# Kernel optimization log

Hardware: AMD Instinct MI355X
Metric: run time of the kernel (lower is better)

Reference implementation:

```python
import jax, jax.numpy as jnp
import numpy as np


def _gcn_conv(x, edge_index, W, b):
    # PyG GCNConv: h = x @ W; out = D^{-1/2}(A+I)D^{-1/2} h + b
    N = x.shape[0]
    src, dst = edge_index[0], edge_index[1]
    # degree with self-loops (edge weights = 1)
    deg = jax.ops.segment_sum(jnp.ones(src.shape[0], x.dtype), dst, num_segments=N) + 1.0
    dis = jax.lax.rsqrt(deg)  # deg >= 1 so finite
    h = x @ W  # [N, F_out]
    norm = dis[src] * dis[dst]  # [E]
    msg = h[src] * norm[:, None]  # [E, F_out] -- dominant memory traffic
    agg = jax.ops.segment_sum(msg, dst, num_segments=N)
    # self-loop contribution: norm_ii = dis_i^2
    out = agg + h * (dis * dis)[:, None] + b
    return out


def setup_inputs() -> dict:
    key = jax.random.key(0)
    k1, k2, k3, k4, k5, k6 = jax.random.split(key, 6)
    N, E = 100000, 1600000
    in_ch, hid, out_ch = 256, 128, 64  # hid = 2*out_channels
    x = jax.random.normal(k1, (N, in_ch), dtype=jnp.float32)
    edge_index = jax.random.randint(k2, (2, E), 0, N, dtype=jnp.int64)
    # Glorot-style init for GCN weights, zero bias (PyG default)
    W1 = jax.random.normal(k3, (in_ch, hid), dtype=jnp.float32) / np.sqrt(in_ch)
    b1 = jnp.zeros((hid,), jnp.float32)
    W2 = jax.random.normal(k4, (hid, out_ch), dtype=jnp.float32) / np.sqrt(hid)
    b2 = jnp.zeros((out_ch,), jnp.float32)
    return {"x": x, "edge_index": edge_index, "W1": W1, "b1": b1, "W2": W2, "b2": b2}


def reference(x, edge_index, W1, b1, W2, b2):
    # Encoder.forward: k=2 layers of activation(GCNConv(x, edge_index))
    h = jax.nn.relu(_gcn_conv(x, edge_index, W1, b1))
    h = jax.nn.relu(_gcn_conv(h, edge_index, W2, b2))
    return h
```

## Files before the change

### kernel.cpp

```cpp
#include <hip/hip_runtime.h>
#include <math.h>

#define THREADS 256
#define HIST_ILP 8
#define EPB_SHIFT 11

static inline int cdiv(long long a, long long b) { return (int)((a + b - 1) / b); }

typedef __attribute__((ext_vector_type(8))) short bf16x8;
typedef __attribute__((ext_vector_type(4))) float f32x4;

__device__ inline unsigned f2bf_rne_u(float f) {
    unsigned u = __builtin_bit_cast(unsigned, f);
    return (u + 0x7FFFu + ((u >> 16) & 1u)) >> 16;
}
__device__ inline float bfu2f(unsigned h) {
    unsigned u = h << 16;
    return __builtin_bit_cast(float, u);
}


__device__ __forceinline__ void bfrag_unit(const float* __restrict__ W, short* __restrict__ frag,
                                           int NCT, int ctks, int lane) {
    int Nn = NCT * 16;
    int ct = ctks % NCT;
    int ks = ctks / NCT;
    int colc = ct * 16 + (lane & 15);
    int kbase = ks * 32 + (lane >> 4) * 8;
    short* base = frag + (size_t)ctks * 1024 + lane * 8;
    #pragma unroll
    for (int j = 0; j < 8; ++j) {
        float v = W[(size_t)(kbase + j) * Nn + colc];
        unsigned h = f2bf_rne_u(v);
        base[j] = (short)h;
        base[512 + j] = (short)f2bf_rne_u(v - bfu2f(h));
    }
}

__device__ __forceinline__ void hist8_body(const int* __restrict__ dst, int* __restrict__ deg8,
                                           int* __restrict__ rank, int E, int N,
                                           int hb, int copy) {
    int* deg = deg8 + (size_t)copy * N;
    const int chi = copy << 28;
    int base = (hb << EPB_SHIFT) + (int)threadIdx.x * HIST_ILP;
    if (base + HIST_ILP - 1 < E) {
        int4 d0 = *(const int4*)(dst + base);
        int4 d1 = *(const int4*)(dst + base + 4);
        int4 r0, r1;
        r0.x = atomicAdd(&deg[d0.x], 1) | chi;
        r0.y = atomicAdd(&deg[d0.y], 1) | chi;
        r0.z = atomicAdd(&deg[d0.z], 1) | chi;
        r0.w = atomicAdd(&deg[d0.w], 1) | chi;
        r1.x = atomicAdd(&deg[d1.x], 1) | chi;
        r1.y = atomicAdd(&deg[d1.y], 1) | chi;
        r1.z = atomicAdd(&deg[d1.z], 1) | chi;
        r1.w = atomicAdd(&deg[d1.w], 1) | chi;
        *(int4*)(rank + base) = r0;
        *(int4*)(rank + base + 4) = r1;
    } else {
        for (int e = base; e < E; ++e) rank[e] = atomicAdd(&deg[dst[e]], 1) | chi;
    }
}

__device__ __forceinline__ void fill_body(const int* __restrict__ src, const int* __restrict__ dst,
                                          const int* __restrict__ rank, const int* __restrict__ rp8,
                                          int* __restrict__ col, int E, int N, int blk) {
    int base = (blk * THREADS + (int)threadIdx.x) * 4;
    if (base + 3 < E) {
        int4 d = *(const int4*)(dst + base);
        int4 r = *(const int4*)(rank + base);
        int4 s = *(const int4*)(src + base);
        col[rp8[(size_t)(((unsigned)r.x) >> 28) * N + d.x] + (r.x & 0x0FFFFFFF)] = s.x;
        col[rp8[(size_t)(((unsigned)r.y) >> 28) * N + d.y] + (r.y & 0x0FFFFFFF)] = s.y;
        col[rp8[(size_t)(((unsigned)r.z) >> 28) * N + d.z] + (r.z & 0x0FFFFFFF)] = s.z;
        col[rp8[(size_t)(((unsigned)r.w) >> 28) * N + d.w] + (r.w & 0x0FFFFFFF)] = s.w;
    } else {
        for (int e = base; e < E; ++e) {
            int r = rank[e];
            col[rp8[(size_t)(((unsigned)r) >> 28) * N + dst[e]] + (r & 0x0FFFFFFF)] = src[e];
        }
    }
}

template<int NCT, int KS>
__device__ __forceinline__ void gemm_body(const float* __restrict__ A, const short* __restrict__ Bfrag,
                                          unsigned short* __restrict__ H, int M, int blk) {
    constexpr int K = KS * 32;
    constexpr int Nn = NCT * 16;
    const int lane = threadIdx.x & 63;
    const int wave = threadIdx.x >> 6;
    const int rowBase = blk * 128 + wave * 32;
    const int kgrp = (lane >> 4) * 8;

    const float* ap0;
    const float* ap1;
    {
        int r0 = rowBase + (lane & 15);      if (r0 >= M) r0 = M - 1;
        int r1 = rowBase + (lane & 15) + 16; if (r1 >= M) r1 = M - 1;
        ap0 = A + (size_t)r0 * K + kgrp;
        ap1 = A + (size_t)r1 * K + kgrp;
    }

    f32x4 acc[2][NCT] = {};

    float4 c00 = *(const float4*)(ap0);
    float4 c01 = *(const float4*)(ap0 + 4);
    float4 c10 = *(const float4*)(ap1);
    float4 c11 = *(const float4*)(ap1 + 4);

    for (int ks = 0; ks < KS; ++ks) {
        float4 n00, n01, n10, n11;
        if (ks + 1 < KS) {
            const float* p0 = ap0 + (size_t)(ks + 1) * 32;
            const float* p1 = ap1 + (size_t)(ks + 1) * 32;
            n00 = *(const float4*)(p0);
            n01 = *(const float4*)(p0 + 4);
            n10 = *(const float4*)(p1);
            n11 = *(const float4*)(p1 + 4);
        }
        bf16x8 ahi[2], alo[2];
        {
            float av0[8] = {c00.x, c00.y, c00.z, c00.w, c01.x, c01.y, c01.z, c01.w};
            float av1[8] = {c10.x, c10.y, c10.z, c10.w, c11.x, c11.y, c11.z, c11.w};
            #pragma unroll
            for (int j = 0; j < 8; ++j) {
                unsigned h0 = f2bf_rne_u(av0[j]);
                ahi[0][j] = (short)h0;
                alo[0][j] = (short)f2bf_rne_u(av0[j] - bfu2f(h0));
                unsigned h1 = f2bf_rne_u(av1[j]);
                ahi[1][j] = (short)h1;
                alo[1][j] = (short)f2bf_rne_u(av1[j] - bfu2f(h1));
            }
        }
        __builtin_amdgcn_s_setprio(1);
        #pragma unroll
        for (int ct = 0; ct < NCT; ++ct) {
            const short* bp = Bfrag + (size_t)(ks * NCT + ct) * 1024 + lane * 8;
            bf16x8 bhi = *(const bf16x8*)bp;
            bf16x8 blo = *(const bf16x8*)(bp + 512);
            #pragma unroll
            for (int t = 0; t < 2; ++t) {
                acc[t][ct] = __builtin_amdgcn_mfma_f32_16x16x32_bf16(ahi[t], bhi, acc[t][ct], 0, 0, 0);
                acc[t][ct] = __builtin_amdgcn_mfma_f32_16x16x32_bf16(ahi[t], blo, acc[t][ct], 0, 0, 0);
                acc[t][ct] = __builtin_amdgcn_mfma_f32_16x16x32_bf16(alo[t], bhi, acc[t][ct], 0, 0, 0);
            }
        }
        __builtin_amdgcn_s_setprio(0);
        c00 = n00; c01 = n01; c10 = n10; c11 = n11;
    }

    const int drow0 = rowBase + (lane >> 4) * 4;
    #pragma unroll
    for (int t = 0; t < 2; ++t) {
        #pragma unroll
        for (int r = 0; r < 4; ++r) {
            int row = drow0 + t * 16 + r;
            if (row < M) {
                unsigned short* hp = H + (size_t)row * Nn + (lane & 15);
                #pragma unroll
                for (int ct = 0; ct < NCT; ++ct)
                    hp[ct * 16] = (unsigned short)f2bf_rne_u(acc[t][ct][r]);
            }
        }
    }
}


__global__ __launch_bounds__(THREADS)
void zero_bfrag_kernel(int* __restrict__ deg8, int total8,
                       const float* __restrict__ W1, short* __restrict__ bf1,
                       const float* __restrict__ W2, short* __restrict__ bf2, int nbZero) {
    int b = (int)blockIdx.x;
    if (b < nbZero) {
        int base = (b * THREADS + (int)threadIdx.x) * 4;
        if (base + 3 < total8) {
            *(int4*)(deg8 + base) = make_int4(0, 0, 0, 0);
        } else {
            for (int i = base; i < total8; ++i) deg8[i] = 0;
        }
    } else {
        int u = (b - nbZero) * 4 + ((int)threadIdx.x >> 6);
        int lane = threadIdx.x & 63;
        if (u < 64) bfrag_unit(W1, bf1, 8, u, lane);
        else if (u < 80) bfrag_unit(W2, bf2, 4, u - 64, lane);
    }
}

__global__ __launch_bounds__(THREADS)
void hist_gemmA_kernel(const int* __restrict__ dst, int* __restrict__ deg8,
                       int* __restrict__ rank, int E, int N,
                       const float* __restrict__ A, const short* __restrict__ Bfrag,
                       unsigned short* __restrict__ H, int M,
                       int nbHist, int nbGemm) {
    int b = (int)blockIdx.x;
    int total = nbHist + nbGemm;
    long long t = (long long)b * nbGemm;
    int gBefore = (int)(t / total);
    bool isG = (((long long)(b + 1) * nbGemm) / total) > gBefore;
    if (isG) gemm_body<8, 8>(A, Bfrag, H, M, gBefore);
    else     hist8_body(dst, deg8, rank, E, N, b - gBefore, b & 7);
}

__global__ __launch_bounds__(THREADS)
void fill_gemmB_kernel(const int* __restrict__ src, const int* __restrict__ dst,
                       const int* __restrict__ rank, const int* __restrict__ rp8,
                       int* __restrict__ col, int E, int N,
                       const float* __restrict__ A, const short* __restrict__ Bfrag,
                       unsigned short* __restrict__ H, int M, int gemmOff,
                       int nbFill, int nbGemm) {
    int b = (int)blockIdx.x;
    int total = nbFill + nbGemm;
    long long t = (long long)b * nbGemm;
    int gBefore = (int)(t / total);
    bool isG = (((long long)(b + 1) * nbGemm) / total) > gBefore;
    if (isG) gemm_body<8, 8>(A, Bfrag, H, M, gemmOff + gBefore);
    else     fill_body(src, dst, rank, rp8, col, E, N, b - gBefore);
}

template<int NCT, int KS>
__global__ __launch_bounds__(THREADS)
void mfma_gemm_bf16out_kernel(const float* __restrict__ A, const short* __restrict__ Bfrag,
                              unsigned short* __restrict__ H, int M) {
    gemm_body<NCT, KS>(A, Bfrag, H, M, (int)blockIdx.x);
}


#define SCAN_BLOCK 256
#define SCAN_ITEMS 4

__global__ __launch_bounds__(SCAN_BLOCK)
void scan_block_kernel(const int* __restrict__ deg8, int* __restrict__ out,
                       int* __restrict__ blockSums, float* __restrict__ dis, int n) {
    __shared__ int sdata[SCAN_BLOCK];
    int base = blockIdx.x * (SCAN_BLOCK * SCAN_ITEMS);
    int tid = threadIdx.x;
    int v[SCAN_ITEMS];
    int sum = 0;
    #pragma unroll
    for (int k = 0; k < SCAN_ITEMS; ++k) {
        int idx = base + tid * SCAN_ITEMS + k;
        int s8 = 0;
        if (idx < n) {
            #pragma unroll
            for (int c = 0; c < 8; ++c) s8 += deg8[(size_t)c * n + idx];
            dis[idx] = rsqrtf((float)s8 + 1.0f);
        }
        v[k] = s8;
        sum += s8;
    }
    sdata[tid] = sum;
    __syncthreads();
    for (int off = 1; off < SCAN_BLOCK; off <<= 1) {
        int t = (tid >= off) ? sdata[tid - off] : 0;
        __syncthreads();
        sdata[tid] += t;
        __syncthreads();
    }
    if (tid == SCAN_BLOCK - 1) blockSums[blockIdx.x] = sdata[SCAN_BLOCK - 1];
    int run = (tid == 0) ? 0 : sdata[tid - 1];
    #pragma unroll
    for (int k = 0; k < SCAN_ITEMS; ++k) {
        int idx = base + tid * SCAN_ITEMS + k;
        if (idx < n) out[idx] = run;
        run += v[k];
    }
}

__global__ __launch_bounds__(SCAN_BLOCK)
void scan_sums_kernel(int* __restrict__ blockSums, int nB) {
    __shared__ int sdata[SCAN_BLOCK];
    int tid = threadIdx.x;
    sdata[tid] = (tid < nB) ? blockSums[tid] : 0;
    __syncthreads();
    for (int off = 1; off < SCAN_BLOCK; off <<= 1) {
        int t = (tid >= off) ? sdata[tid - off] : 0;
        __syncthreads();
        sdata[tid] += t;
        __syncthreads();
    }
    int excl = (tid == 0) ? 0 : sdata[tid - 1];
    if (tid < nB) blockSums[tid] = excl;
}

__global__ __launch_bounds__(SCAN_BLOCK)
void scan_add_rp8_kernel(int* __restrict__ rowptr, const int* __restrict__ blockSums,
                         const int* __restrict__ deg8, int* __restrict__ rp8,
                         int n, int E) {
    int base = blockIdx.x * (SCAN_BLOCK * SCAN_ITEMS);
    int add = blockSums[blockIdx.x];
    #pragma unroll
    for (int k = 0; k < SCAN_ITEMS; ++k) {
        int idx = base + threadIdx.x * SCAN_ITEMS + k;
        if (idx < n) {
            int val = rowptr[idx] + add;
            rowptr[idx] = val;
            int run = val;
            #pragma unroll
            for (int c = 0; c < 8; ++c) {
                rp8[(size_t)c * n + idx] = run;
                run += deg8[(size_t)c * n + idx];
            }
        }
    }
    if (blockIdx.x == 0 && threadIdx.x == 0) rowptr[n] = E;
}


__global__ __launch_bounds__(THREADS)
void gather_bf16_128_kernel(const unsigned short* __restrict__ g, const int* __restrict__ col,
                            const int* __restrict__ rowptr, const float* __restrict__ dis,
                            const float* __restrict__ bias, float* __restrict__ out, int N) {
    constexpr int F = 128;
    int wid = (int)((blockIdx.x * (long long)blockDim.x + threadIdx.x) >> 6);
    wid = __builtin_amdgcn_readfirstlane(wid);
    const int lane = threadIdx.x & 63;
    if (wid >= N) return;
    const float di = dis[wid];
    const int loff = lane * 2;

    float acc0 = 0.0f, acc1 = 0.0f;

    auto loadrow = [&](int s) -> unsigned {
        return *(const unsigned*)(g + (size_t)s * F + loff);
    };
    auto addconv = [&](unsigned u, float w) {
        acc0 += w * bfu2f(u & 0xFFFFu);
        acc1 += w * __builtin_bit_cast(float, u & 0xFFFF0000u);
    };

    addconv(loadrow(wid), di);

    int start = __builtin_amdgcn_readfirstlane(rowptr[wid]);
    int end   = __builtin_amdgcn_readfirstlane(rowptr[wid + 1]);
    const int* c = col + start;
    int rem = end - start;

    if (rem >= 4) {
        int s0 = __builtin_amdgcn_readfirstlane(c[0]);
        int s1 = __builtin_amdgcn_readfirstlane(c[1]);
        int s2 = __builtin_amdgcn_readfirstlane(c[2]);
        int s3 = __builtin_amdgcn_readfirstlane(c[3]);
        float w0 = dis[s0], w1 = dis[s1], w2 = dis[s2], w3 = dis[s3];
        unsigned u0 = loadrow(s0), u1 = loadrow(s1), u2 = loadrow(s2), u3 = loadrow(s3);
        c += 4; rem -= 4;
        while (rem >= 4) {
            int t0 = __builtin_amdgcn_readfirstlane(c[0]);
            int t1 = __builtin_amdgcn_readfirstlane(c[1]);
            int t2 = __builtin_amdgcn_readfirstlane(c[2]);
            int t3 = __builtin_amdgcn_readfirstlane(c[3]);
            float x0 = dis[t0], x1 = dis[t1], x2 = dis[t2], x3 = dis[t3];
            unsigned v0 = loadrow(t0), v1 = loadrow(t1), v2 = loadrow(t2), v3 = loadrow(t3);
            addconv(u0, w0); addconv(u1, w1); addconv(u2, w2); addconv(u3, w3);
            u0 = v0; u1 = v1; u2 = v2; u3 = v3;
            w0 = x0; w1 = x1; w2 = x2; w3 = x3;
            c += 4; rem -= 4;
        }
        addconv(u0, w0); addconv(u1, w1); addconv(u2, w2); addconv(u3, w3);
    }
    while (rem > 0) {
        int s = __builtin_amdgcn_readfirstlane(c[0]);
        addconv(loadrow(s), dis[s]);
        ++c; --rem;
    }

    float* orow = out + (size_t)wid * F + loff;
    float v0 = di * acc0 + bias[loff];
    float v1 = di * acc1 + bias[loff + 1];
    *(float2*)orow = make_float2(fmaxf(v0, 0.0f), fmaxf(v1, 0.0f));
}

__global__ __launch_bounds__(THREADS)
void gather_pair64_kernel(const unsigned short* __restrict__ g, const int* __restrict__ col,
                          const int* __restrict__ rowptr, const float* __restrict__ dis,
                          const float* __restrict__ bias, float* __restrict__ out, int N) {
    int wid = (int)((blockIdx.x * (long long)blockDim.x + threadIdx.x) >> 6);
    if (wid >= N) return;
    const int lane = threadIdx.x & 63;
    const int half = lane >> 5;
    const int cc = lane & 31;
    const float di = dis[wid];

    float acc0 = 0.0f, acc1 = 0.0f;

    auto loadrow = [&](int s) -> unsigned {
        return *(const unsigned*)(g + (size_t)s * 64 + cc * 2);
    };
    auto addconv = [&](unsigned u, float w) {
        acc0 += w * bfu2f(u & 0xFFFFu);
        acc1 += w * __builtin_bit_cast(float, u & 0xFFFF0000u);
    };

    addconv(loadrow(wid), half ? 0.0f : di);

    int start = rowptr[wid], end = rowptr[wid + 1];
    int j = start + half;
    int cnt = (j < end) ? ((end - j + 1) >> 1) : 0;

    if (cnt >= 4) {
        int s0 = col[j], s1 = col[j + 2], s2 = col[j + 4], s3 = col[j + 6];
        float w0 = dis[s0], w1 = dis[s1], w2 = dis[s2], w3 = dis[s3];
        unsigned u0 = loadrow(s0), u1 = loadrow(s1), u2 = loadrow(s2), u3 = loadrow(s3);
        j += 8; cnt -= 4;
        while (cnt >= 4) {
            int t0 = col[j], t1 = col[j + 2], t2 = col[j + 4], t3 = col[j + 6];
            float x0 = dis[t0], x1 = dis[t1], x2 = dis[t2], x3 = dis[t3];
            unsigned v0 = loadrow(t0), v1 = loadrow(t1), v2 = loadrow(t2), v3 = loadrow(t3);
            addconv(u0, w0); addconv(u1, w1); addconv(u2, w2); addconv(u3, w3);
            u0 = v0; u1 = v1; u2 = v2; u3 = v3;
            w0 = x0; w1 = x1; w2 = x2; w3 = x3;
            j += 8; cnt -= 4;
        }
        addconv(u0, w0); addconv(u1, w1); addconv(u2, w2); addconv(u3, w3);
    }
    while (cnt > 0) {
        int s = col[j];
        addconv(loadrow(s), dis[s]);
        j += 2; --cnt;
    }

    acc0 += __shfl_xor(acc0, 32);
    acc1 += __shfl_xor(acc1, 32);

    if (half == 0) {
        float v0 = fmaxf(di * acc0 + bias[cc * 2 + 0], 0.0f);
        float v1 = fmaxf(di * acc1 + bias[cc * 2 + 1], 0.0f);
        *(float2*)(out + (size_t)wid * 64 + cc * 2) = make_float2(v0, v1);
    }
}


#define BM 64
#define BN 64
#define BK 16

__global__ __launch_bounds__(THREADS)
void sgemm_kernel(const float* __restrict__ A, const float* __restrict__ B,
                  float* __restrict__ C, int M, int N, int K) {
    __shared__ float As[BK][BM + 1];
    __shared__ float Bs[BK][BN + 1];

    const int tid = threadIdx.x;
    const int tr = tid / 16;
    const int tc = tid % 16;
    const int rowBase = blockIdx.y * BM;
    const int colBase = blockIdx.x * BN;

    float acc[4][4] = {};

    for (int k0 = 0; k0 < K; k0 += BK) {
        #pragma unroll
        for (int i = tid; i < BM * BK; i += THREADS) {
            int r = i / BK, c = i % BK;
            int gr = rowBase + r;
            As[c][r] = (gr < M) ? A[(size_t)gr * K + k0 + c] : 0.0f;
        }
        #pragma unroll
        for (int i = tid; i < BK * BN; i += THREADS) {
            int r = i / BN, c = i % BN;
            Bs[r][c] = B[(size_t)(k0 + r) * N + colBase + c];
        }
        __syncthreads();

        #pragma unroll
        for (int k = 0; k < BK; ++k) {
            float a[4], b[4];
            #pragma unroll
            for (int m = 0; m < 4; ++m) a[m] = As[k][tr * 4 + m];
            #pragma unroll
            for (int n = 0; n < 4; ++n) b[n] = Bs[k][tc * 4 + n];
            #pragma unroll
            for (int m = 0; m < 4; ++m)
                #pragma unroll
                for (int n = 0; n < 4; ++n)
                    acc[m][n] += a[m] * b[n];
        }
        __syncthreads();
    }

    #pragma unroll
    for (int m = 0; m < 4; ++m) {
        int gr = rowBase + tr * 4 + m;
        if (gr >= M) continue;
        #pragma unroll
        for (int n = 0; n < 4; ++n) {
            C[(size_t)gr * N + colBase + tc * 4 + n] = acc[m][n];
        }
    }
}

__global__ __launch_bounds__(THREADS)
void init_agg_kernel(const float* __restrict__ h, const float* __restrict__ dis,
                     float* __restrict__ agg, int N, int F) {
    int i = blockIdx.x * blockDim.x + threadIdx.x;
    int total = N * (F / 4);
    if (i >= total) return;
    int node = i / (F / 4);
    float d = dis[node];
    float w = d * d;
    float4 v = ((const float4*)h)[i];
    v.x *= w; v.y *= w; v.z *= w; v.w *= w;
    ((float4*)agg)[i] = v;
}

__global__ __launch_bounds__(THREADS)
void edge_scatter_kernel(const float* __restrict__ h, const int* __restrict__ src,
                         const int* __restrict__ dst, const float* __restrict__ dis,
                         float* __restrict__ agg, int E, int F) {
    int lanesPerEdge = F / 4;
    int tid = blockIdx.x * blockDim.x + threadIdx.x;
    int e = tid / lanesPerEdge;
    int c = tid % lanesPerEdge;
    if (e >= E) return;
    int s = src[e];
    int d = dst[e];
    float w = dis[s] * dis[d];
    float4 hv = ((const float4*)(h + (size_t)s * F))[c];
    float* ap = agg + (size_t)d * F + (size_t)c * 4;
    atomicAdd(ap + 0, hv.x * w);
    atomicAdd(ap + 1, hv.y * w);
    atomicAdd(ap + 2, hv.z * w);
    atomicAdd(ap + 3, hv.w * w);
}

__global__ __launch_bounds__(THREADS)
void finalize_kernel(const float* __restrict__ agg, const float* __restrict__ b,
                     float* __restrict__ out, int N, int F) {
    int i = blockIdx.x * blockDim.x + threadIdx.x;
    int total = N * (F / 4);
    if (i >= total) return;
    int c4 = i % (F / 4);
    float4 bv = ((const float4*)b)[c4];
    float4 v = ((const float4*)agg)[i];
    v.x = fmaxf(v.x + bv.x, 0.0f);
    v.y = fmaxf(v.y + bv.y, 0.0f);
    v.z = fmaxf(v.z + bv.z, 0.0f);
    v.w = fmaxf(v.w + bv.w, 0.0f);
    ((float4*)out)[i] = v;
}

__global__ __launch_bounds__(THREADS)
void fdeg_kernel(const int* __restrict__ dst, float* __restrict__ deg, int E) {
    int i = blockIdx.x * blockDim.x + threadIdx.x;
    if (i < E) atomicAdd(&deg[dst[i]], 1.0f);
}

__global__ __launch_bounds__(THREADS)
void fdis_kernel(float* __restrict__ deg, int N) {
    int i = blockIdx.x * blockDim.x + threadIdx.x;
    if (i < N) deg[i] = rsqrtf(deg[i] + 1.0f);
}


extern "C" void kernel_launch(void* const* d_in, const int* in_sizes, int n_in,
                              void* d_out, int out_size, void* d_ws, size_t ws_size,
                              hipStream_t stream) {
    const float* x  = (const float*)d_in[0];
    const int*   ei = (const int*)d_in[1];
    const float* W1 = (const float*)d_in[2];
    const float* b1 = (const float*)d_in[3];
    const float* W2 = (const float*)d_in[4];
    const float* b2 = (const float*)d_in[5];

    const int E    = in_sizes[1] / 2;
    const int hid  = in_sizes[3];
    const int outc = in_sizes[5];
    const int inc  = in_sizes[2] / hid;
    const int N    = in_sizes[0] / inc;

    const int* src = ei;
    const int* dst = ei + E;
    float* out = (float*)d_out;
    char* ws = (char*)d_ws;

    auto al = [](size_t v) { return (v + 255) & ~(size_t)255; };
    size_t o_dis  = 0;
    size_t o_deg8 = al(o_dis + (size_t)N * 4);
    size_t o_rp   = al(o_deg8 + (size_t)N * 32);
    size_t o_rp8  = al(o_rp + ((size_t)N + 1) * 4);
    size_t o_bs   = al(o_rp8 + (size_t)N * 32);
    size_t o_col  = al(o_bs + 4096);
    size_t o_rank = al(o_col + (size_t)E * 4);
    size_t o_bf1  = al(o_rank + (size_t)E * 4);
    size_t o_bf2  = al(o_bf1 + 131072);
    size_t o_G    = al(o_bf2 + 32768);
    size_t o_B    = al(o_G + (size_t)N * hid * 2);
    size_t need   = o_B + (size_t)N * hid * 4;

    if (ws_size >= need && N <= SCAN_BLOCK * SCAN_BLOCK * SCAN_ITEMS &&
        hid == 128 && outc == 64 && inc == 256 && E < (1 << 28)) {
        float* dis    = (float*)(ws + o_dis);
        int*   deg8   = (int*)(ws + o_deg8);
        int*   rowptr = (int*)(ws + o_rp);
        int*   rp8    = (int*)(ws + o_rp8);
        int*   bsums  = (int*)(ws + o_bs);
        int*   col    = (int*)(ws + o_col);
        int*   rank   = (int*)(ws + o_rank);
        short* bf1    = (short*)(ws + o_bf1);
        short* bf2    = (short*)(ws + o_bf2);
        unsigned short* gbuf = (unsigned short*)(ws + o_G);
        float* out1   = (float*)(ws + o_B);

        const int nbZero  = cdiv((long long)N * 8, 4 * THREADS);
        const int nbHist  = cdiv(E, THREADS * HIST_ILP);
        const int nbGemm1 = cdiv(N, 128);
        const int nbGemmA = (nbGemm1 * 3) / 5;
        const int nbGemmB = nbGemm1 - nbGemmA;
        const int nbFill  = cdiv(E, 4 * THREADS);

        zero_bfrag_kernel<<<nbZero + 20, THREADS, 0, stream>>>(deg8, N * 8, W1, bf1, W2, bf2, nbZero);

        hist_gemmA_kernel<<<nbHist + nbGemmA, THREADS, 0, stream>>>(
            dst, deg8, rank, E, N, x, bf1, gbuf, N, nbHist, nbGemmA);

        int nB = cdiv(N, SCAN_BLOCK * SCAN_ITEMS);
        scan_block_kernel<<<nB, SCAN_BLOCK, 0, stream>>>(deg8, rowptr, bsums, dis, N);
        scan_sums_kernel<<<1, SCAN_BLOCK, 0, stream>>>(bsums, nB);
        scan_add_rp8_kernel<<<nB, SCAN_BLOCK, 0, stream>>>(rowptr, bsums, deg8, rp8, N, E);

        fill_gemmB_kernel<<<nbFill + nbGemmB, THREADS, 0, stream>>>(
            src, dst, rank, rp8, col, E, N, x, bf1, gbuf, N, nbGemmA, nbFill, nbGemmB);

        gather_bf16_128_kernel<<<cdiv((long long)N * 64, THREADS), THREADS, 0, stream>>>(
            gbuf, col, rowptr, dis, b1, out1, N);

        mfma_gemm_bf16out_kernel<4, 4><<<cdiv(N, 128), THREADS, 0, stream>>>(out1, bf2, gbuf, N);
        gather_pair64_kernel<<<cdiv((long long)N * 64, THREADS), THREADS, 0, stream>>>(
            gbuf, col, rowptr, dis, b2, out, N);
        return;
    }

    float* dis = (float*)ws;
    size_t off1 = ((size_t)N * 4 + 255) & ~(size_t)255;
    float* h1 = (float*)(ws + off1);
    size_t off2 = off1 + ((((size_t)N * hid * 4) + 255) & ~(size_t)255);
    float* agg1 = (float*)(ws + off2);
    float* h2   = agg1;
    float* agg2 = agg1 + (size_t)N * outc;

    hipMemsetAsync(dis, 0, (size_t)N * 4, stream);
    fdeg_kernel<<<cdiv(E, THREADS), THREADS, 0, stream>>>(dst, dis, E);
    fdis_kernel<<<cdiv(N, THREADS), THREADS, 0, stream>>>(dis, N);

    {
        dim3 grid(hid / BN, cdiv(N, BM));
        sgemm_kernel<<<grid, THREADS, 0, stream>>>(x, W1, h1, N, hid, inc);
    }
    init_agg_kernel<<<cdiv((long long)N * hid / 4, THREADS), THREADS, 0, stream>>>(h1, dis, agg1, N, hid);
    edge_scatter_kernel<<<cdiv((long long)E * (hid / 4), THREADS), THREADS, 0, stream>>>(
        h1, src, dst, dis, agg1, E, hid);
    finalize_kernel<<<cdiv((long long)N * hid / 4, THREADS), THREADS, 0, stream>>>(agg1, b1, h1, N, hid);

    {
        dim3 grid(outc / BN, cdiv(N, BM));
        sgemm_kernel<<<grid, THREADS, 0, stream>>>(h1, W2, h2, N, outc, hid);
    }
    init_agg_kernel<<<cdiv((long long)N * outc / 4, THREADS), THREADS, 0, stream>>>(h2, dis, agg2, N, outc);
    edge_scatter_kernel<<<cdiv((long long)E * (outc / 4), THREADS), THREADS, 0, stream>>>(
        h2, src, dst, dis, agg2, E, outc);
    finalize_kernel<<<cdiv((long long)N * outc / 4, THREADS), THREADS, 0, stream>>>(agg2, b2, out, N, outc);
}
```

Measured before the change: 290.1 us.

## Drop 8-way replicated degree histogram and use paired-half gather for layer one

Replaces the eight replicated degree counters (each with its own partial rowptr) with a single degree array, which simplifies the scan, scan-add and CSR fill kernels and removes the rp8 buffer. The 128-wide layer-one gather now uses the same two-half-wave scheme as the 64-wide kernel, with each half handling alternate edges, loading 4 bf16 per lane and combining the halves with a shuffle. The GEMM split between the hist and fill kernels is also rebalanced. The risk is heavier atomic contention on a single degree counter per node, and the gather's per-lane column index loads replace the earlier scalar readfirstlane loads.

```diff
diff --git a/kernel.cpp b/kernel.cpp
--- a/kernel.cpp
+++ b/kernel.cpp
@@ -37,48 +37,43 @@
     }
 }
 
-__device__ __forceinline__ void hist8_body(const int* __restrict__ dst, int* __restrict__ deg8,
-                                           int* __restrict__ rank, int E, int N,
-                                           int hb, int copy) {
-    int* deg = deg8 + (size_t)copy * N;
-    const int chi = copy << 28;
+__device__ __forceinline__ void hist_body8(const int* __restrict__ dst, int* __restrict__ deg,
+                                           int* __restrict__ rank, int E, int hb) {
     int base = (hb << EPB_SHIFT) + (int)threadIdx.x * HIST_ILP;
     if (base + HIST_ILP - 1 < E) {
         int4 d0 = *(const int4*)(dst + base);
         int4 d1 = *(const int4*)(dst + base + 4);
         int4 r0, r1;
-        r0.x = atomicAdd(&deg[d0.x], 1) | chi;
-        r0.y = atomicAdd(&deg[d0.y], 1) | chi;
-        r0.z = atomicAdd(&deg[d0.z], 1) | chi;
-        r0.w = atomicAdd(&deg[d0.w], 1) | chi;
-        r1.x = atomicAdd(&deg[d1.x], 1) | chi;
-        r1.y = atomicAdd(&deg[d1.y], 1) | chi;
-        r1.z = atomicAdd(&deg[d1.z], 1) | chi;
-        r1.w = atomicAdd(&deg[d1.w], 1) | chi;
+        r0.x = atomicAdd(&deg[d0.x], 1);
+        r0.y = atomicAdd(&deg[d0.y], 1);
+        r0.z = atomicAdd(&deg[d0.z], 1);
+        r0.w = atomicAdd(&deg[d0.w], 1);
+        r1.x = atomicAdd(&deg[d1.x], 1);
+        r1.y = atomicAdd(&deg[d1.y], 1);
+        r1.z = atomicAdd(&deg[d1.z], 1);
+        r1.w = atomicAdd(&deg[d1.w], 1);
         *(int4*)(rank + base) = r0;
         *(int4*)(rank + base + 4) = r1;
     } else {
-        for (int e = base; e < E; ++e) rank[e] = atomicAdd(&deg[dst[e]], 1) | chi;
+        for (int e = base; e < E; ++e) rank[e] = atomicAdd(&deg[dst[e]], 1);
     }
 }
 
 __device__ __forceinline__ void fill_body(const int* __restrict__ src, const int* __restrict__ dst,
-                                          const int* __restrict__ rank, const int* __restrict__ rp8,
-                                          int* __restrict__ col, int E, int N, int blk) {
+                                          const int* __restrict__ rank, const int* __restrict__ rowptr,
+                                          int* __restrict__ col, int E, int blk) {
     int base = (blk * THREADS + (int)threadIdx.x) * 4;
     if (base + 3 < E) {
         int4 d = *(const int4*)(dst + base);
         int4 r = *(const int4*)(rank + base);
         int4 s = *(const int4*)(src + base);
-        col[rp8[(size_t)(((unsigned)r.x) >> 28) * N + d.x] + (r.x & 0x0FFFFFFF)] = s.x;
-        col[rp8[(size_t)(((unsigned)r.y) >> 28) * N + d.y] + (r.y & 0x0FFFFFFF)] = s.y;
-        col[rp8[(size_t)(((unsigned)r.z) >> 28) * N + d.z] + (r.z & 0x0FFFFFFF)] = s.z;
-        col[rp8[(size_t)(((unsigned)r.w) >> 28) * N + d.w] + (r.w & 0x0FFFFFFF)] = s.w;
+        col[rowptr[d.x] + r.x] = s.x;
+        col[rowptr[d.y] + r.y] = s.y;
+        col[rowptr[d.z] + r.z] = s.z;
+        col[rowptr[d.w] + r.w] = s.w;
     } else {
-        for (int e = base; e < E; ++e) {
-            int r = rank[e];
-            col[rp8[(size_t)(((unsigned)r) >> 28) * N + dst[e]] + (r & 0x0FFFFFFF)] = src[e];
-        }
+        for (int e = base; e < E; ++e)
+            col[rowptr[dst[e]] + rank[e]] = src[e];
     }
 }
 
@@ -167,16 +162,16 @@
 
 
 __global__ __launch_bounds__(THREADS)
-void zero_bfrag_kernel(int* __restrict__ deg8, int total8,
+void zero_bfrag_kernel(int* __restrict__ deg, int N,
                        const float* __restrict__ W1, short* __restrict__ bf1,
                        const float* __restrict__ W2, short* __restrict__ bf2, int nbZero) {
     int b = (int)blockIdx.x;
     if (b < nbZero) {
         int base = (b * THREADS + (int)threadIdx.x) * 4;
-        if (base + 3 < total8) {
-            *(int4*)(deg8 + base) = make_int4(0, 0, 0, 0);
+        if (base + 3 < N) {
+            *(int4*)(deg + base) = make_int4(0, 0, 0, 0);
         } else {
-            for (int i = base; i < total8; ++i) deg8[i] = 0;
+            for (int i = base; i < N; ++i) deg[i] = 0;
         }
     } else {
         int u = (b - nbZero) * 4 + ((int)threadIdx.x >> 6);
@@ -187,8 +182,8 @@
 }
 
 __global__ __launch_bounds__(THREADS)
-void hist_gemmA_kernel(const int* __restrict__ dst, int* __restrict__ deg8,
-                       int* __restrict__ rank, int E, int N,
+void hist_gemmA_kernel(const int* __restrict__ dst, int* __restrict__ deg,
+                       int* __restrict__ rank, int E,
                        const float* __restrict__ A, const short* __restrict__ Bfrag,
                        unsigned short* __restrict__ H, int M,
                        int nbHist, int nbGemm) {
@@ -198,13 +193,13 @@
     int gBefore = (int)(t / total);
     bool isG = (((long long)(b + 1) * nbGemm) / total) > gBefore;
     if (isG) gemm_body<8, 8>(A, Bfrag, H, M, gBefore);
-    else     hist8_body(dst, deg8, rank, E, N, b - gBefore, b & 7);
+    else     hist_body8(dst, deg, rank, E, b - gBefore);
 }
 
 __global__ __launch_bounds__(THREADS)
 void fill_gemmB_kernel(const int* __restrict__ src, const int* __restrict__ dst,
-                       const int* __restrict__ rank, const int* __restrict__ rp8,
-                       int* __restrict__ col, int E, int N,
+                       const int* __restrict__ rank, const int* __restrict__ rowptr,
+                       int* __restrict__ col, int E,
                        const float* __restrict__ A, const short* __restrict__ Bfrag,
                        unsigned short* __restrict__ H, int M, int gemmOff,
                        int nbFill, int nbGemm) {
@@ -214,7 +209,7 @@
     int gBefore = (int)(t / total);
     bool isG = (((long long)(b + 1) * nbGemm) / total) > gBefore;
     if (isG) gemm_body<8, 8>(A, Bfrag, H, M, gemmOff + gBefore);
-    else     fill_body(src, dst, rank, rp8, col, E, N, b - gBefore);
+    else     fill_body(src, dst, rank, rowptr, col, E, b - gBefore);
 }
 
 template<int NCT, int KS>
@@ -229,7 +224,7 @@
 #define SCAN_ITEMS 4
 
 __global__ __launch_bounds__(SCAN_BLOCK)
-void scan_block_kernel(const int* __restrict__ deg8, int* __restrict__ out,
+void scan_block_kernel(const int* __restrict__ in, int* __restrict__ out,
                        int* __restrict__ blockSums, float* __restrict__ dis, int n) {
     __shared__ int sdata[SCAN_BLOCK];
     int base = blockIdx.x * (SCAN_BLOCK * SCAN_ITEMS);
@@ -239,14 +234,9 @@
     #pragma unroll
     for (int k = 0; k < SCAN_ITEMS; ++k) {
         int idx = base + tid * SCAN_ITEMS + k;
-        int s8 = 0;
-        if (idx < n) {
-            #pragma unroll
-            for (int c = 0; c < 8; ++c) s8 += deg8[(size_t)c * n + idx];
-            dis[idx] = rsqrtf((float)s8 + 1.0f);
-        }
-        v[k] = s8;
-        sum += s8;
+        v[k] = (idx < n) ? in[idx] : 0;
+        if (idx < n) dis[idx] = rsqrtf((float)v[k] + 1.0f);
+        sum += v[k];
     }
     sdata[tid] = sum;
     __syncthreads();
@@ -283,90 +273,83 @@
 }
 
 __global__ __launch_bounds__(SCAN_BLOCK)
-void scan_add_rp8_kernel(int* __restrict__ rowptr, const int* __restrict__ blockSums,
-                         const int* __restrict__ deg8, int* __restrict__ rp8,
-                         int n, int E) {
+void scan_add_kernel(int* __restrict__ out, const int* __restrict__ blockSums,
+                     int n, int E) {
     int base = blockIdx.x * (SCAN_BLOCK * SCAN_ITEMS);
     int add = blockSums[blockIdx.x];
     #pragma unroll
     for (int k = 0; k < SCAN_ITEMS; ++k) {
         int idx = base + threadIdx.x * SCAN_ITEMS + k;
-        if (idx < n) {
-            int val = rowptr[idx] + add;
-            rowptr[idx] = val;
-            int run = val;
-            #pragma unroll
-            for (int c = 0; c < 8; ++c) {
-                rp8[(size_t)c * n + idx] = run;
-                run += deg8[(size_t)c * n + idx];
-            }
-        }
-    }
-    if (blockIdx.x == 0 && threadIdx.x == 0) rowptr[n] = E;
-}
-
-
-__global__ __launch_bounds__(THREADS)
-void gather_bf16_128_kernel(const unsigned short* __restrict__ g, const int* __restrict__ col,
-                            const int* __restrict__ rowptr, const float* __restrict__ dis,
-                            const float* __restrict__ bias, float* __restrict__ out, int N) {
-    constexpr int F = 128;
+        if (idx < n) out[idx] += add;
+    }
+    if (blockIdx.x == 0 && threadIdx.x == 0) out[n] = E;
+}
+
+
+__global__ __launch_bounds__(THREADS)
+void gather_pair128_kernel(const unsigned short* __restrict__ g, const int* __restrict__ col,
+                           const int* __restrict__ rowptr, const float* __restrict__ dis,
+                           const float* __restrict__ bias, float* __restrict__ out, int N) {
     int wid = (int)((blockIdx.x * (long long)blockDim.x + threadIdx.x) >> 6);
-    wid = __builtin_amdgcn_readfirstlane(wid);
+    if (wid >= N) return;
     const int lane = threadIdx.x & 63;
-    if (wid >= N) return;
+    const int half = lane >> 5;
+    const int cc = lane & 31;
     const float di = dis[wid];
-    const int loff = lane * 2;
-
-    float acc0 = 0.0f, acc1 = 0.0f;
-
-    auto loadrow = [&](int s) -> unsigned {
-        return *(const unsigned*)(g + (size_t)s * F + loff);
+
+    float a0 = 0, a1 = 0, a2 = 0, a3 = 0;
+
+    auto loadrow = [&](int s) -> uint2 {
+        return *(const uint2*)(g + (size_t)s * 128 + cc * 4);
     };
-    auto addconv = [&](unsigned u, float w) {
-        acc0 += w * bfu2f(u & 0xFFFFu);
-        acc1 += w * __builtin_bit_cast(float, u & 0xFFFF0000u);
+    auto addconv = [&](uint2 u, float w) {
+        a0 += w * bfu2f(u.x & 0xFFFFu);
+        a1 += w * __builtin_bit_cast(float, u.x & 0xFFFF0000u);
+        a2 += w * bfu2f(u.y & 0xFFFFu);
+        a3 += w * __builtin_bit_cast(float, u.y & 0xFFFF0000u);
     };
 
-    addconv(loadrow(wid), di);
-
-    int start = __builtin_amdgcn_readfirstlane(rowptr[wid]);
-    int end   = __builtin_amdgcn_readfirstlane(rowptr[wid + 1]);
-    const int* c = col + start;
-    int rem = end - start;
-
-    if (rem >= 4) {
-        int s0 = __builtin_amdgcn_readfirstlane(c[0]);
-        int s1 = __builtin_amdgcn_readfirstlane(c[1]);
-        int s2 = __builtin_amdgcn_readfirstlane(c[2]);
-        int s3 = __builtin_amdgcn_readfirstlane(c[3]);
+    if (half == 0) addconv(loadrow(wid), di);
+
+    int start = rowptr[wid], end = rowptr[wid + 1];
+    int j = start + half;
+    int cnt = (j < end) ? ((end - j + 1) >> 1) : 0;
+
+    if (cnt >= 4) {
+        int s0 = col[j], s1 = col[j + 2], s2 = col[j + 4], s3 = col[j + 6];
         float w0 = dis[s0], w1 = dis[s1], w2 = dis[s2], w3 = dis[s3];
-        unsigned u0 = loadrow(s0), u1 = loadrow(s1), u2 = loadrow(s2), u3 = loadrow(s3);
-        c += 4; rem -= 4;
-        while (rem >= 4) {
-            int t0 = __builtin_amdgcn_readfirstlane(c[0]);
-            int t1 = __builtin_amdgcn_readfirstlane(c[1]);
-            int t2 = __builtin_amdgcn_readfirstlane(c[2]);
-            int t3 = __builtin_amdgcn_readfirstlane(c[3]);
+        uint2 u0 = loadrow(s0), u1 = loadrow(s1), u2 = loadrow(s2), u3 = loadrow(s3);
+        j += 8; cnt -= 4;
+        while (cnt >= 4) {
+            int t0 = col[j], t1 = col[j + 2], t2 = col[j + 4], t3 = col[j + 6];
             float x0 = dis[t0], x1 = dis[t1], x2 = dis[t2], x3 = dis[t3];
-            unsigned v0 = loadrow(t0), v1 = loadrow(t1), v2 = loadrow(t2), v3 = loadrow(t3);
+            uint2 v0 = loadrow(t0), v1 = loadrow(t1), v2 = loadrow(t2), v3 = loadrow(t3);
             addconv(u0, w0); addconv(u1, w1); addconv(u2, w2); addconv(u3, w3);
             u0 = v0; u1 = v1; u2 = v2; u3 = v3;
             w0 = x0; w1 = x1; w2 = x2; w3 = x3;
-            c += 4; rem -= 4;
+            j += 8; cnt -= 4;
         }
         addconv(u0, w0); addconv(u1, w1); addconv(u2, w2); addconv(u3, w3);
     }
-    while (rem > 0) {
-        int s = __builtin_amdgcn_readfirstlane(c[0]);
+    while (cnt > 0) {
+        int s = col[j];
         addconv(loadrow(s), dis[s]);
-        ++c; --rem;
-    }
-
-    float* orow = out + (size_t)wid * F + loff;
-    float v0 = di * acc0 + bias[loff];
-    float v1 = di * acc1 + bias[loff + 1];
-    *(float2*)orow = make_float2(fmaxf(v0, 0.0f), fmaxf(v1, 0.0f));
+        j += 2; --cnt;
+    }
+
+    a0 += __shfl_xor(a0, 32);
+    a1 += __shfl_xor(a1, 32);
+    a2 += __shfl_xor(a2, 32);
+    a3 += __shfl_xor(a3, 32);
+
+    if (half == 0) {
+        float4 v;
+        v.x = fmaxf(di * a0 + bias[cc * 4 + 0], 0.0f);
+        v.y = fmaxf(di * a1 + bias[cc * 4 + 1], 0.0f);
+        v.z = fmaxf(di * a2 + bias[cc * 4 + 2], 0.0f);
+        v.w = fmaxf(di * a3 + bias[cc * 4 + 3], 0.0f);
+        *(float4*)(out + (size_t)wid * 128 + cc * 4) = v;
+    }
 }
 
 __global__ __launch_bounds__(THREADS)
@@ -380,17 +363,17 @@
     const int cc = lane & 31;
     const float di = dis[wid];
 
-    float acc0 = 0.0f, acc1 = 0.0f;
+    float a0 = 0, a1 = 0;
 
     auto loadrow = [&](int s) -> unsigned {
         return *(const unsigned*)(g + (size_t)s * 64 + cc * 2);
     };
     auto addconv = [&](unsigned u, float w) {
-        acc0 += w * bfu2f(u & 0xFFFFu);
-        acc1 += w * __builtin_bit_cast(float, u & 0xFFFF0000u);
+        a0 += w * bfu2f(u & 0xFFFFu);
+        a1 += w * __builtin_bit_cast(float, u & 0xFFFF0000u);
     };
 
-    addconv(loadrow(wid), half ? 0.0f : di);
+    if (half == 0) addconv(loadrow(wid), di);
 
     int start = rowptr[wid], end = rowptr[wid + 1];
     int j = start + half;
@@ -418,12 +401,12 @@
         j += 2; --cnt;
     }
 
-    acc0 += __shfl_xor(acc0, 32);
-    acc1 += __shfl_xor(acc1, 32);
+    a0 += __shfl_xor(a0, 32);
+    a1 += __shfl_xor(a1, 32);
 
     if (half == 0) {
-        float v0 = fmaxf(di * acc0 + bias[cc * 2 + 0], 0.0f);
-        float v1 = fmaxf(di * acc1 + bias[cc * 2 + 1], 0.0f);
+        float v0 = fmaxf(di * a0 + bias[cc * 2 + 0], 0.0f);
+        float v1 = fmaxf(di * a1 + bias[cc * 2 + 1], 0.0f);
         *(float2*)(out + (size_t)wid * 64 + cc * 2) = make_float2(v0, v1);
     }
 }
@@ -574,10 +557,9 @@
 
     auto al = [](size_t v) { return (v + 255) & ~(size_t)255; };
     size_t o_dis  = 0;
-    size_t o_deg8 = al(o_dis + (size_t)N * 4);
-    size_t o_rp   = al(o_deg8 + (size_t)N * 32);
-    size_t o_rp8  = al(o_rp + ((size_t)N + 1) * 4);
-    size_t o_bs   = al(o_rp8 + (size_t)N * 32);
+    size_t o_deg  = al(o_dis + (size_t)N * 4);
+    size_t o_rp   = al(o_deg + (size_t)N * 4);
+    size_t o_bs   = al(o_rp + ((size_t)N + 1) * 4);
     size_t o_col  = al(o_bs + 4096);
     size_t o_rank = al(o_col + (size_t)E * 4);
     size_t o_bf1  = al(o_rank + (size_t)E * 4);
@@ -587,11 +569,10 @@
     size_t need   = o_B + (size_t)N * hid * 4;
 
     if (ws_size >= need && N <= SCAN_BLOCK * SCAN_BLOCK * SCAN_ITEMS &&
-        hid == 128 && outc == 64 && inc == 256 && E < (1 << 28)) {
+        hid == 128 && outc == 64 && inc == 256) {
         float* dis    = (float*)(ws + o_dis);
-        int*   deg8   = (int*)(ws + o_deg8);
+        int*   deg    = (int*)(ws + o_deg);
         int*   rowptr = (int*)(ws + o_rp);
-        int*   rp8    = (int*)(ws + o_rp8);
         int*   bsums  = (int*)(ws + o_bs);
         int*   col    = (int*)(ws + o_col);
         int*   rank   = (int*)(ws + o_rank);
@@ -600,27 +581,27 @@
         unsigned short* gbuf = (unsigned short*)(ws + o_G);
         float* out1   = (float*)(ws + o_B);
 
-        const int nbZero  = cdiv((long long)N * 8, 4 * THREADS);
+        const int nbZero  = cdiv(N, 4 * THREADS);
         const int nbHist  = cdiv(E, THREADS * HIST_ILP);
         const int nbGemm1 = cdiv(N, 128);
-        const int nbGemmA = (nbGemm1 * 3) / 5;
+        const int nbGemmA = (nbGemm1 * 5) / 9;
         const int nbGemmB = nbGemm1 - nbGemmA;
         const int nbFill  = cdiv(E, 4 * THREADS);
 
-        zero_bfrag_kernel<<<nbZero + 20, THREADS, 0, stream>>>(deg8, N * 8, W1, bf1, W2, bf2, nbZero);
+        zero_bfrag_kernel<<<nbZero + 20, THREADS, 0, stream>>>(deg, N, W1, bf1, W2, bf2, nbZero);
 
         hist_gemmA_kernel<<<nbHist + nbGemmA, THREADS, 0, stream>>>(
-            dst, deg8, rank, E, N, x, bf1, gbuf, N, nbHist, nbGemmA);
+            dst, deg, rank, E, x, bf1, gbuf, N, nbHist, nbGemmA);
 
         int nB = cdiv(N, SCAN_BLOCK * SCAN_ITEMS);
-        scan_block_kernel<<<nB, SCAN_BLOCK, 0, stream>>>(deg8, rowptr, bsums, dis, N);
+        scan_block_kernel<<<nB, SCAN_BLOCK, 0, stream>>>(deg, rowptr, bsums, dis, N);
         scan_sums_kernel<<<1, SCAN_BLOCK, 0, stream>>>(bsums, nB);
-        scan_add_rp8_kernel<<<nB, SCAN_BLOCK, 0, stream>>>(rowptr, bsums, deg8, rp8, N, E);
+        scan_add_kernel<<<nB, SCAN_BLOCK, 0, stream>>>(rowptr, bsums, N, E);
 
         fill_gemmB_kernel<<<nbFill + nbGemmB, THREADS, 0, stream>>>(
-            src, dst, rank, rp8, col, E, N, x, bf1, gbuf, N, nbGemmA, nbFill, nbGemmB);
-
-        gather_bf16_128_kernel<<<cdiv((long long)N * 64, THREADS), THREADS, 0, stream>>>(
+            src, dst, rank, rowptr, col, E, x, bf1, gbuf, N, nbGemmA, nbFill, nbGemmB);
+
+        gather_pair128_kernel<<<cdiv((long long)N * 64, THREADS), THREADS, 0, stream>>>(
             gbuf, col, rowptr, dis, b1, out1, N);
 
         mfma_gemm_bf16out_kernel<4, 4><<<cdiv(N, 128), THREADS, 0, stream>>>(out1, bf2, gbuf, N);
```

Result: faster. 282.0 us (-2.8%).
